# Kernel optimization log

Measured on AMD Instinct MI355X. Metric: run time of the kernel, lower is better.

The kernel has to match this reference:

```python
import jax, jax.numpy as jnp
import numpy as np

C_IN = 256
C_OUT = 256
NUM_HEADS = 4
C_HEAD = C_OUT // NUM_HEADS  # 64
ALPHA = 0.2
NEG_FILL = -9e15


def setup_inputs() -> dict:
    key = jax.random.key(0)
    k1, k2, k3, k4, k5 = jax.random.split(key, 5)
    B, N = 1, 4096
    node_feats = jax.random.normal(k1, (B, N, C_IN), dtype=jnp.float32)
    adj_matrix = jax.random.randint(k2, (B, N, N), 0, 2, dtype=jnp.int32)
    # xavier_uniform with gain=1.414 on projection weight (fan_in=C_IN, fan_out=C_OUT)
    lim_w = 1.414 * np.sqrt(6.0 / (C_IN + C_OUT))
    W = jax.random.uniform(k3, (C_IN, C_OUT), dtype=jnp.float32, minval=-lim_w, maxval=lim_w)
    b = jnp.zeros((C_OUT,), dtype=jnp.float32)
    lim_a = 1.414 * np.sqrt(6.0 / (NUM_HEADS + 2 * C_HEAD))
    a = jax.random.uniform(k4, (NUM_HEADS, 2 * C_HEAD), dtype=jnp.float32, minval=-lim_a, maxval=lim_a)
    return {"node_feats": node_feats, "adj_matrix": adj_matrix, "W": W, "b": b, "a": a}


def reference(node_feats, adj_matrix, W, b, a):
    B, N, _ = node_feats.shape
    # linear projection -> (B, N, H, C_HEAD)
    feats = (node_feats @ W + b).reshape(B, N, NUM_HEADS, C_HEAD)
    # attention logit for edge (i -> j): a_src . h_i + a_dst . h_j, per head
    a_src, a_dst = a[:, :C_HEAD], a[:, C_HEAD:]
    src = jnp.einsum('bnhc,hc->bnh', feats, a_src)  # indexed by row i
    dst = jnp.einsum('bnhc,hc->bnh', feats, a_dst)  # indexed by col j
    logits = src[:, :, None, :] + dst[:, None, :, :]  # (B, N, N, H)
    logits = jnp.where(logits >= 0, logits, ALPHA * logits)  # LeakyReLU(0.2)
    attn = jnp.where(adj_matrix[..., None] == 1, logits, NEG_FILL)
    probs = jax.nn.softmax(attn, axis=2)  # softmax over source nodes j
    out = jnp.einsum('bijh,bjhc->bihc', probs, feats)
    return out.reshape(B, N, NUM_HEADS * C_HEAD)  # concat heads
```

## Files before the change

kernel.cpp:

```cpp
#include <hip/hip_runtime.h>

#define NN 4096
#define C 256
#define NH 4
#define CH 64
#define JSPLIT 16
#define JSLICE (NN / JSPLIT)
#define NJT (JSLICE / 32)

typedef float f32x4 __attribute__((ext_vector_type(4)));
typedef __bf16 b16x8 __attribute__((ext_vector_type(8)));
typedef unsigned short u16x8 __attribute__((ext_vector_type(8)));
typedef unsigned int u32x4 __attribute__((ext_vector_type(4)));
typedef _Float16 f16x2 __attribute__((ext_vector_type(2)));

__device__ inline float fast_exp2(float x) {
#if __has_builtin(__builtin_amdgcn_exp2f)
  return __builtin_amdgcn_exp2f(x);
#else
  return exp2f(x);
#endif
}

__device__ inline unsigned pack2bf(float f0, float f1) {
  unsigned u0 = __float_as_uint(f0) + 0x8000u;
  unsigned u1 = __float_as_uint(f1) + 0x8000u;
  return __builtin_amdgcn_perm(u1, u0, 0x07060302u);
}

__device__ inline unsigned cvtpk(float f0, float f1) {
  unsigned r;
  asm("v_cvt_pk_bf16_f32 %0, %1, %2" : "=v"(r) : "v"(f0), "v"(f1));
  return r;
}

__global__ __launch_bounds__(256) void k_prep(
    const float* __restrict__ X, const float* __restrict__ W,
    unsigned short* __restrict__ Xbf, unsigned short* __restrict__ WT) {
  const int b = blockIdx.x, t = threadIdx.x;
  if (b < 1024) {
    const int idx = b * 256 + t;
    const float4 v = ((const float4*)X)[idx];
    uint2 st;
    st.x = pack2bf(v.x, v.y);
    st.y = pack2bf(v.z, v.w);
    ((uint2*)Xbf)[idx] = st;
  } else {
    const int c = b - 1024;
    const float w = W[(size_t)t * C + c];
    WT[(size_t)c * C + t] = (unsigned short)((__float_as_uint(w) + 0x8000u) >> 16);
  }
}

__global__ __launch_bounds__(256) void k_feats(
    const unsigned short* __restrict__ Xbf, const unsigned short* __restrict__ WT,
    const float* __restrict__ bias, const float* __restrict__ av,
    const int* __restrict__ adj, unsigned char* __restrict__ packed,
    unsigned short* __restrict__ F, float2* __restrict__ srcAB,
    float* __restrict__ Ed) {
  if (blockIdx.x >= 256) {
    const int idx = (blockIdx.x - 256) * 256 + threadIdx.x;
    const int4 a0 = *(const int4*)(adj + (size_t)idx * 8);
    const int4 a1 = *(const int4*)(adj + (size_t)idx * 8 + 4);
    unsigned m = 0;
    m |= (a0.x != 0) ? 1u : 0u;   m |= (a0.y != 0) ? 2u : 0u;
    m |= (a0.z != 0) ? 4u : 0u;   m |= (a0.w != 0) ? 8u : 0u;
    m |= (a1.x != 0) ? 16u : 0u;  m |= (a1.y != 0) ? 32u : 0u;
    m |= (a1.z != 0) ? 64u : 0u;  m |= (a1.w != 0) ? 128u : 0u;
    packed[idx] = (unsigned char)m;
    return;
  }
  const int i0 = blockIdx.x * 16;
  const int h = threadIdx.x >> 6;
  const int lane = threadIdx.x & 63;
  const int q = lane >> 4, n = lane & 15;
  const int c0 = h * CH;
  const float LOG2E = 1.4426950408889634f;

  const f32x4 zero = {0.f, 0.f, 0.f, 0.f};
  f32x4 acc[4];
#pragma unroll
  for (int g = 0; g < 4; ++g) acc[g] = zero;

  const unsigned short* ap = Xbf + (size_t)(i0 + n) * C + q * 8;
#pragma unroll
  for (int kt = 0; kt < 8; ++kt) {
    const b16x8 aF = __builtin_bit_cast(b16x8, *(const u16x8*)(ap + kt * 32));
#pragma unroll
    for (int g = 0; g < 4; ++g) {
      const b16x8 bF = __builtin_bit_cast(b16x8,
          *(const u16x8*)(WT + (size_t)(c0 + g * 16 + n) * C + kt * 32 + q * 8));
      acc[g] = __builtin_amdgcn_mfma_f32_16x16x32_bf16(aF, bF, acc[g], 0, 0, 0);
    }
  }

  float fb[4][4], asv[4], adv[4];
#pragma unroll
  for (int g = 0; g < 4; ++g) {
    const float bs = bias[c0 + g * 16 + n];
    asv[g] = av[h * 128 + g * 16 + n];
    adv[g] = av[h * 128 + 64 + g * 16 + n];
#pragma unroll
    for (int r = 0; r < 4; ++r) fb[g][r] = acc[g][r] + bs;
  }
  const int jt = i0 >> 5, half = (i0 >> 4) & 1;
  const int qp = half * 2 + (q >> 1);
#pragma unroll
  for (int g = 0; g < 4; ++g) {
    uint2 st;
    st.x = pack2bf(fb[g][0], fb[g][1]);
    st.y = pack2bf(fb[g][2], fb[g][3]);
    *(uint2*)(F + ((size_t)((jt * NH + h) * 4 + g)) * 512 + (qp * 16 + n) * 8 + 4 * (q & 1)) = st;
  }
#pragma unroll
  for (int r = 0; r < 4; ++r) {
    float p = 0.f, d = 0.f;
#pragma unroll
    for (int g = 0; g < 4; ++g) {
      p = fmaf(fb[g][r], asv[g], p);
      d = fmaf(fb[g][r], adv[g], d);
    }
#pragma unroll
    for (int m = 1; m < 16; m <<= 1) {
      p += __shfl_xor(p, m);
      d += __shfl_xor(d, m);
    }
    if (n == 0) {
      const int row = i0 + q * 4 + r;
      const float dL = d * LOG2E;
      Ed[(size_t)h * NN + row] = fast_exp2(dL);
      Ed[(size_t)NH * NN + (size_t)h * NN + row] = fast_exp2(0.2f * dL);
      const float x = p + 16.0f;
      const float m2 = fmaxf(x, 0.2f * x) * LOG2E;
      srcAB[(size_t)row * NH + h] = make_float2(
          fast_exp2(fmaf(p, LOG2E, -m2)),
          fast_exp2(fmaf(0.2f * p, LOG2E, -m2)));
    }
  }
}

__global__ __launch_bounds__(256, 4) void k_attn(
    const unsigned char* __restrict__ packed,
    const unsigned short* __restrict__ F,
    const float2* __restrict__ srcAB, const float* __restrict__ Ed,
    _Float16* __restrict__ pacc, float* __restrict__ lpart) {
  const int slice = blockIdx.x;
  const int i0 = blockIdx.y * 32;
  const int h = threadIdx.x >> 6;
  const int lane = threadIdx.x & 63;
  const int q = lane >> 4, n = lane & 15;
  const int jbase = slice * JSLICE;

  const int r0 = i0 + n, r1 = i0 + 16 + n;
  const float2 ab0 = srcAB[(size_t)r0 * NH + h];
  const float2 ab1 = srcAB[(size_t)r1 * NH + h];

  const f32x4 zero = {0.f, 0.f, 0.f, 0.f};
  f32x4 acc0[4], acc1[4], lacc0 = zero, lacc1 = zero;
#pragma unroll
  for (int g = 0; g < 4; ++g) { acc0[g] = zero; acc1[g] = zero; }

  u16x8 ou;
#pragma unroll
  for (int jj = 0; jj < 8; ++jj) ou[jj] = 0x3F80;
  const b16x8 ones = __builtin_bit_cast(b16x8, ou);

  const uint2 m20 = *(const uint2*)(packed + (size_t)r0 * 512 + (jbase >> 3) + q * 8);
  const uint2 m21 = *(const uint2*)(packed + (size_t)r1 * 512 + (jbase >> 3) + q * 8);

  const float* pa = Ed + (size_t)h * NN + jbase;
  const float* pb = pa + (size_t)NH * NN;
  const unsigned short* fp = F + ((size_t)((jbase >> 5) * NH + h) * 4) * 512 + lane * 8;

#pragma unroll
  for (int a = 0; a < 4; ++a) {
#pragma unroll
    for (int b = 0; b < 2; ++b) {
      const int jt = a * 2 + b;
      b16x8 bF[4];
#pragma unroll
      for (int g = 0; g < 4; ++g)
        bF[g] = __builtin_bit_cast(b16x8,
            *(const u16x8*)(fp + (size_t)(jt * NH * 4 + g) * 512));

      const int w0 = b ? (int)m20.y : (int)m20.x;
      const int w1 = b ? (int)m21.y : (int)m21.x;
      const unsigned Mb0 = (unsigned(__shfl(w0, a * 16 + n)) >> (q * 8)) & 0xffu;
      const unsigned Mb1 = (unsigned(__shfl(w1, a * 16 + n)) >> (q * 8)) & 0xffu;

      const int off = jt * 32 + q * 8;
      const f32x4 eA[2] = { *(const f32x4*)(pa + off), *(const f32x4*)(pa + off + 4) };
      const f32x4 eB[2] = { *(const f32x4*)(pb + off), *(const f32x4*)(pb + off + 4) };

      u32x4 pk0, pk1;
#pragma unroll
      for (int hf = 0; hf < 2; ++hf) {
        const f32x4 xa0 = eA[hf] * ab0.x;
        const f32x4 xb0 = eB[hf] * ab0.y;
        const f32x4 xa1 = eA[hf] * ab1.x;
        const f32x4 xb1 = eB[hf] * ab1.y;
        float e0[4], e1[4];
#pragma unroll
        for (int t2 = 0; t2 < 4; ++t2) {
          const unsigned bit = 1u << (hf * 4 + t2);
          e0[t2] = (Mb0 & bit) ? fmaxf(xa0[t2], xb0[t2]) : 0.f;
          e1[t2] = (Mb1 & bit) ? fmaxf(xa1[t2], xb1[t2]) : 0.f;
        }
        pk0[hf * 2]     = cvtpk(e0[0], e0[1]);
        pk0[hf * 2 + 1] = cvtpk(e0[2], e0[3]);
        pk1[hf * 2]     = cvtpk(e1[0], e1[1]);
        pk1[hf * 2 + 1] = cvtpk(e1[2], e1[3]);
      }
      const b16x8 E0 = __builtin_bit_cast(b16x8, pk0);
      const b16x8 E1 = __builtin_bit_cast(b16x8, pk1);
#pragma unroll
      for (int g = 0; g < 4; ++g) {
        acc0[g] = __builtin_amdgcn_mfma_f32_16x16x32_bf16(E0, bF[g], acc0[g], 0, 0, 0);
        acc1[g] = __builtin_amdgcn_mfma_f32_16x16x32_bf16(E1, bF[g], acc1[g], 0, 0, 0);
      }
      lacc0 = __builtin_amdgcn_mfma_f32_16x16x32_bf16(E0, ones, lacc0, 0, 0, 0);
      lacc1 = __builtin_amdgcn_mfma_f32_16x16x32_bf16(E1, ones, lacc1, 0, 0, 0);
    }
  }

#pragma unroll
  for (int g = 0; g < 4; ++g)
#pragma unroll
    for (int r = 0; r < 4; ++r) {
      const int col = h * CH + g * 16 + n;
      pacc[((size_t)slice * NN + i0 + q * 4 + r) * C + col] = (_Float16)acc0[g][r];
      pacc[((size_t)slice * NN + i0 + 16 + q * 4 + r) * C + col] = (_Float16)acc1[g][r];
    }
  if (n == 0) {
#pragma unroll
    for (int r = 0; r < 4; ++r) {
      lpart[((size_t)slice * NN + i0 + q * 4 + r) * NH + h] = lacc0[r];
      lpart[((size_t)slice * NN + i0 + 16 + q * 4 + r) * NH + h] = lacc1[r];
    }
  }
}

__global__ __launch_bounds__(256) void k_final(
    const _Float16* __restrict__ pacc, const float* __restrict__ lpart,
    float* __restrict__ out) {
  const int t = threadIdx.x;
  const int row = blockIdx.x * 2 + (t >> 7);
  const int tc = t & 127;
  const int c2 = tc * 2;
  const int h = tc >> 5;
  float l = 0.f, sa0 = 0.f, sa1 = 0.f;
#pragma unroll
  for (int sp = 0; sp < JSPLIT; ++sp) {
    l += lpart[((size_t)sp * NN + row) * NH + h];
    const f16x2 v = *(const f16x2*)(pacc + ((size_t)sp * NN + row) * C + c2);
    sa0 += (float)v[0];
    sa1 += (float)v[1];
  }
  const float rl = 1.0f / l;
  *(float2*)(out + (size_t)row * C + c2) = make_float2(sa0 * rl, sa1 * rl);
}

extern "C" void kernel_launch(void* const* d_in, const int* in_sizes, int n_in,
                              void* d_out, int out_size, void* d_ws, size_t ws_size,
                              hipStream_t stream) {
  const float* nf   = (const float*)d_in[0];
  const int* adj    = (const int*)d_in[1];
  const float* W    = (const float*)d_in[2];
  const float* bias = (const float*)d_in[3];
  const float* av   = (const float*)d_in[4];
  float* out = (float*)d_out;

  char* ws = (char*)d_ws;
  unsigned char* packed  = (unsigned char*)ws;
  unsigned short* Xbf    = (unsigned short*)(ws + (2u << 20));
  unsigned short* WT     = (unsigned short*)(ws + (4u << 20));
  unsigned short* F      = (unsigned short*)(ws + (4u << 20) + (256u << 10));
  float2* srcAB = (float2*)(ws + (6u << 20) + (256u << 10));
  float* Ed     = (float*)(ws + (6u << 20) + (384u << 10));
  float* lpart  = (float*)(ws + (6u << 20) + (512u << 10));
  _Float16* pacc = (_Float16*)(ws + (8u << 20));

  k_prep<<<1280, 256, 0, stream>>>(nf, W, Xbf, WT);
  k_feats<<<8448, 256, 0, stream>>>(Xbf, WT, bias, av, adj, packed, F, srcAB, Ed);
  dim3 g2(JSPLIT, NN / 32);
  k_attn<<<g2, 256, 0, stream>>>(packed, F, srcAB, Ed, pacc, lpart);
  k_final<<<NN / 2, 256, 0, stream>>>(pacc, lpart, out);
}
```

Measured before the change: 142.7 us.

## Restructure attention tiling: fewer j-slices, 16-row blocks, stage Ed in LDS

Halves the number of j-slices so each block covers 512 source nodes, and drops from 32 to 16 destination rows per block, so each wave now computes one 16-row MFMA tile. The per-head exp factors Ed for the slice are staged into shared memory once per block, and the loop reads them from there instead of from global memory. Halving JSPLIT also halves the partial-sum traffic that k_final has to reduce. In exchange, F features are reused across only 16 rows instead of 32, which doubles F loads per output. The block count stays the same but the inner loop runs 16 iterations per block.

Measured after the change: 140.8 us. No clear change (-1.3%).

```diff
diff --git a/kernel.cpp b/kernel.cpp
--- a/kernel.cpp
+++ b/kernel.cpp
@@ -4,7 +4,7 @@
 #define C 256
 #define NH 4
 #define CH 64
-#define JSPLIT 16
+#define JSPLIT 8
 #define JSLICE (NN / JSPLIT)
 #define NJT (JSLICE / 32)
 
@@ -144,83 +144,79 @@
     const unsigned short* __restrict__ F,
     const float2* __restrict__ srcAB, const float* __restrict__ Ed,
     _Float16* __restrict__ pacc, float* __restrict__ lpart) {
+  __shared__ float sEd[NH * 2 * JSLICE];
+
   const int slice = blockIdx.x;
-  const int i0 = blockIdx.y * 32;
-  const int h = threadIdx.x >> 6;
-  const int lane = threadIdx.x & 63;
+  const int i0 = blockIdx.y * 16;
+  const int tid = threadIdx.x;
+  const int h = tid >> 6;
+  const int lane = tid & 63;
   const int q = lane >> 4, n = lane & 15;
   const int jbase = slice * JSLICE;
 
-  const int r0 = i0 + n, r1 = i0 + 16 + n;
+  {
+#pragma unroll
+    for (int v = 0; v < 4; ++v) {
+      const int idx = v * 256 + lane * 4;
+      const int pl = idx >> 9, j = idx & 511;
+      const float4 vv = *(const float4*)(Ed + (size_t)pl * NH * NN
+                                         + (size_t)h * NN + jbase + j);
+      *(float4*)(&sEd[h * 1024 + idx]) = vv;
+    }
+  }
+
+  const int r0 = i0 + n;
   const float2 ab0 = srcAB[(size_t)r0 * NH + h];
-  const float2 ab1 = srcAB[(size_t)r1 * NH + h];
 
   const f32x4 zero = {0.f, 0.f, 0.f, 0.f};
-  f32x4 acc0[4], acc1[4], lacc0 = zero, lacc1 = zero;
-#pragma unroll
-  for (int g = 0; g < 4; ++g) { acc0[g] = zero; acc1[g] = zero; }
+  f32x4 acc[4], lacc = zero;
+#pragma unroll
+  for (int g = 0; g < 4; ++g) acc[g] = zero;
 
   u16x8 ou;
 #pragma unroll
   for (int jj = 0; jj < 8; ++jj) ou[jj] = 0x3F80;
   const b16x8 ones = __builtin_bit_cast(b16x8, ou);
 
-  const uint2 m20 = *(const uint2*)(packed + (size_t)r0 * 512 + (jbase >> 3) + q * 8);
-  const uint2 m21 = *(const uint2*)(packed + (size_t)r1 * 512 + (jbase >> 3) + q * 8);
-
-  const float* pa = Ed + (size_t)h * NN + jbase;
-  const float* pb = pa + (size_t)NH * NN;
+  const u32x4 m4 = *(const u32x4*)(packed + (size_t)r0 * 512 + (jbase >> 3) + q * 16);
+
+  const float* sB = &sEd[h * 1024];
   const unsigned short* fp = F + ((size_t)((jbase >> 5) * NH + h) * 4) * 512 + lane * 8;
 
-#pragma unroll
-  for (int a = 0; a < 4; ++a) {
-#pragma unroll
-    for (int b = 0; b < 2; ++b) {
-      const int jt = a * 2 + b;
-      b16x8 bF[4];
-#pragma unroll
-      for (int g = 0; g < 4; ++g)
-        bF[g] = __builtin_bit_cast(b16x8,
-            *(const u16x8*)(fp + (size_t)(jt * NH * 4 + g) * 512));
-
-      const int w0 = b ? (int)m20.y : (int)m20.x;
-      const int w1 = b ? (int)m21.y : (int)m21.x;
-      const unsigned Mb0 = (unsigned(__shfl(w0, a * 16 + n)) >> (q * 8)) & 0xffu;
-      const unsigned Mb1 = (unsigned(__shfl(w1, a * 16 + n)) >> (q * 8)) & 0xffu;
-
-      const int off = jt * 32 + q * 8;
-      const f32x4 eA[2] = { *(const f32x4*)(pa + off), *(const f32x4*)(pa + off + 4) };
-      const f32x4 eB[2] = { *(const f32x4*)(pb + off), *(const f32x4*)(pb + off + 4) };
-
-      u32x4 pk0, pk1;
-#pragma unroll
-      for (int hf = 0; hf < 2; ++hf) {
-        const f32x4 xa0 = eA[hf] * ab0.x;
-        const f32x4 xb0 = eB[hf] * ab0.y;
-        const f32x4 xa1 = eA[hf] * ab1.x;
-        const f32x4 xb1 = eB[hf] * ab1.y;
-        float e0[4], e1[4];
-#pragma unroll
-        for (int t2 = 0; t2 < 4; ++t2) {
-          const unsigned bit = 1u << (hf * 4 + t2);
-          e0[t2] = (Mb0 & bit) ? fmaxf(xa0[t2], xb0[t2]) : 0.f;
-          e1[t2] = (Mb1 & bit) ? fmaxf(xa1[t2], xb1[t2]) : 0.f;
-        }
-        pk0[hf * 2]     = cvtpk(e0[0], e0[1]);
-        pk0[hf * 2 + 1] = cvtpk(e0[2], e0[3]);
-        pk1[hf * 2]     = cvtpk(e1[0], e1[1]);
-        pk1[hf * 2 + 1] = cvtpk(e1[2], e1[3]);
+  __syncthreads();
+
+#pragma unroll
+  for (int jt = 0; jt < NJT; ++jt) {
+    const unsigned Mb =
+        (unsigned(__shfl((int)m4[jt & 3], (jt >> 2) * 16 + n)) >> (q * 8)) & 0xffu;
+
+    const int off = jt * 32 + q * 8;
+    const f32x4 eA[2] = { *(const f32x4*)(sB + off), *(const f32x4*)(sB + off + 4) };
+    const f32x4 eB[2] = { *(const f32x4*)(sB + JSLICE + off),
+                          *(const f32x4*)(sB + JSLICE + off + 4) };
+
+    u32x4 pk;
+#pragma unroll
+    for (int hf = 0; hf < 2; ++hf) {
+      const f32x4 xa = eA[hf] * ab0.x;
+      const f32x4 xb = eB[hf] * ab0.y;
+      float e[4];
+#pragma unroll
+      for (int t2 = 0; t2 < 4; ++t2) {
+        const unsigned bit = 1u << (hf * 4 + t2);
+        e[t2] = (Mb & bit) ? fmaxf(xa[t2], xb[t2]) : 0.f;
       }
-      const b16x8 E0 = __builtin_bit_cast(b16x8, pk0);
-      const b16x8 E1 = __builtin_bit_cast(b16x8, pk1);
-#pragma unroll
-      for (int g = 0; g < 4; ++g) {
-        acc0[g] = __builtin_amdgcn_mfma_f32_16x16x32_bf16(E0, bF[g], acc0[g], 0, 0, 0);
-        acc1[g] = __builtin_amdgcn_mfma_f32_16x16x32_bf16(E1, bF[g], acc1[g], 0, 0, 0);
-      }
-      lacc0 = __builtin_amdgcn_mfma_f32_16x16x32_bf16(E0, ones, lacc0, 0, 0, 0);
-      lacc1 = __builtin_amdgcn_mfma_f32_16x16x32_bf16(E1, ones, lacc1, 0, 0, 0);
-    }
+      pk[hf * 2]     = cvtpk(e[0], e[1]);
+      pk[hf * 2 + 1] = cvtpk(e[2], e[3]);
+    }
+    const b16x8 E = __builtin_bit_cast(b16x8, pk);
+#pragma unroll
+    for (int g = 0; g < 4; ++g) {
+      const b16x8 bF = __builtin_bit_cast(b16x8,
+          *(const u16x8*)(fp + (size_t)(jt * NH * 4 + g) * 512));
+      acc[g] = __builtin_amdgcn_mfma_f32_16x16x32_bf16(E, bF, acc[g], 0, 0, 0);
+    }
+    lacc = __builtin_amdgcn_mfma_f32_16x16x32_bf16(E, ones, lacc, 0, 0, 0);
   }
 
 #pragma unroll
@@ -228,15 +224,12 @@
 #pragma unroll
     for (int r = 0; r < 4; ++r) {
       const int col = h * CH + g * 16 + n;
-      pacc[((size_t)slice * NN + i0 + q * 4 + r) * C + col] = (_Float16)acc0[g][r];
-      pacc[((size_t)slice * NN + i0 + 16 + q * 4 + r) * C + col] = (_Float16)acc1[g][r];
+      pacc[((size_t)slice * NN + i0 + q * 4 + r) * C + col] = (_Float16)acc[g][r];
     }
   if (n == 0) {
 #pragma unroll
-    for (int r = 0; r < 4; ++r) {
-      lpart[((size_t)slice * NN + i0 + q * 4 + r) * NH + h] = lacc0[r];
-      lpart[((size_t)slice * NN + i0 + 16 + q * 4 + r) * NH + h] = lacc1[r];
-    }
+    for (int r = 0; r < 4; ++r)
+      lpart[((size_t)slice * NN + i0 + q * 4 + r) * NH + h] = lacc[r];
   }
 }
 
@@ -282,7 +275,7 @@
 
   k_prep<<<1280, 256, 0, stream>>>(nf, W, Xbf, WT);
   k_feats<<<8448, 256, 0, stream>>>(Xbf, WT, bias, av, adj, packed, F, srcAB, Ed);
-  dim3 g2(JSPLIT, NN / 32);
+  dim3 g2(JSPLIT, NN / 16);
   k_attn<<<g2, 256, 0, stream>>>(packed, F, srcAB, Ed, pacc, lpart);
   k_final<<<NN / 2, 256, 0, stream>>>(pacc, lpart, out);
 }
```
